# Kernel optimization log

Measured on AMD Instinct MI355X. Metric: run time of the kernel, lower is better.

The kernel has to match this reference:

```python
import jax, jax.numpy as jnp
import numpy as np

NUM_LAYER = 6
NUM_HEADS = 1
NEG_INF = -1e9


def setup_inputs() -> dict:
    key = jax.random.key(0)
    ks = jax.random.split(key, 8)
    bs, C, N = 8, 128, 2048
    H0 = (jax.random.uniform(ks[0], (bs, N, N)) < 0.2).astype(jnp.float32)
    vertex_feat = jax.random.normal(ks[1], (bs, C, N), dtype=jnp.float32)
    edge_feat = jax.random.normal(ks[2], (bs, C, N), dtype=jnp.float32)
    s = 1.0 / np.sqrt(C)  # Conv1d(k=1) default init scale
    Wq = jax.random.uniform(ks[3], (C, C), minval=-s, maxval=s, dtype=jnp.float32)
    bq = jax.random.uniform(ks[4], (C,), minval=-s, maxval=s, dtype=jnp.float32)
    Wk = jax.random.uniform(ks[5], (C, C), minval=-s, maxval=s, dtype=jnp.float32)
    bk = jax.random.uniform(ks[6], (C,), minval=-s, maxval=s, dtype=jnp.float32)
    return {"H0": H0, "vertex_feat": vertex_feat, "edge_feat": edge_feat,
            "Wq": Wq, "bq": bq, "Wk": Wk, "bk": bk, "it": 4}


def reference(H0, vertex_feat, edge_feat, Wq, bq, Wk, bk, it):
    bs, N, _ = H0.shape
    C = Wq.shape[0]
    head = NUM_HEADS
    dh = C // head
    # Conv1d kernel_size=1 == pointwise linear over channel dim
    Q = (jnp.einsum('oc,bcn->bon', Wq, vertex_feat) + bq[None, :, None]).reshape(bs, head, dh, N)
    K = (jnp.einsum('oc,bcn->bon', Wk, edge_feat) + bk[None, :, None]).reshape(bs, head, dh, N)
    att = jnp.einsum('bhco,bhci->bhoi', Q, K) / np.sqrt(dh)  # [bs,h,N,N]
    mask = jnp.where(H0 > 0, 0.0, NEG_INF)                   # masked_fill(1-H0)
    score = jax.nn.sigmoid(att + mask[:, None]).sum(axis=1) / head  # [bs,N,N]
    # mask_score, choice='topk': keep top-k scores per row
    k = round(N * 0.1 * (NUM_LAYER - 1 - it))
    topk_vals = jax.lax.top_k(score, k)[0]          # [bs,N,k]
    a_min = topk_vals[..., -1:]                     # k-th largest per row
    W = jnp.where(score >= a_min, score, 0.0)
    H = jnp.where(W > 0, H0, 0.0)
    # degree-normalization matrices (diag_embed of 1/deg, inf -> 0)
    deg_E = H.sum(axis=1)   # [bs,N] edge degrees
    deg_V = H.sum(axis=2)   # [bs,N] vertex degrees
    De_n_1 = jax.vmap(jnp.diag)(jnp.where(deg_E != 0, 1.0 / deg_E, 0.0))
    Dv_n_1 = jax.vmap(jnp.diag)(jnp.where(deg_V != 0, 1.0 / deg_V, 0.0))
    # edge weights: L2-normalized column sums of W (F.normalize, eps=1e-12)
    W_edge = W.sum(axis=1)
    nrm = jnp.maximum(jnp.linalg.norm(W_edge, axis=1, keepdims=True), 1e-12)
    W_edge = (W_edge / nrm)[:, :, None]  # [bs,N,1]
    return H, W, De_n_1, Dv_n_1, W_edge
```

## Files before the change

kernel.cpp:

```cpp
#include <hip/hip_runtime.h>
#include <math.h>

#define NUM_LAYER 6

typedef __attribute__((ext_vector_type(8))) short short8;
typedef __attribute__((ext_vector_type(4))) float f32x4;
typedef unsigned short u16;

__device__ __forceinline__ void split3(float x, u16& h, u16& m, u16& l) {
  unsigned ux = __float_as_uint(x);
  h = (u16)(ux >> 16);
  float r1 = x - __uint_as_float(ux & 0xFFFF0000u);
  unsigned u1 = __float_as_uint(r1);
  m = (u16)(u1 >> 16);
  float r2 = r1 - __uint_as_float(u1 & 0xFFFF0000u);
  l = (u16)(__float_as_uint(r2) >> 16);
}

__global__ __launch_bounds__(256) void qk_gemm_split(
    const float* __restrict__ Wq, const float* __restrict__ bq,
    const float* __restrict__ vf,
    const float* __restrict__ Wk, const float* __restrict__ bk,
    const float* __restrict__ ef,
    u16* __restrict__ Qh, u16* __restrict__ Qm, u16* __restrict__ Ql,
    u16* __restrict__ Kh, u16* __restrict__ Km, u16* __restrict__ Kl,
    int C, int N, int bs) {
  int which = (int)blockIdx.y >= bs;
  int b = (int)blockIdx.y - (which ? bs : 0);
  const float* Wm = which ? Wk : Wq;
  const float* bias = which ? bk : bq;
  const float* X = (which ? ef : vf) + (size_t)b * C * N;
  u16* Ph = which ? Kh : Qh;
  u16* Pm = which ? Km : Qm;
  u16* Pl = which ? Kl : Ql;
  int n0 = blockIdx.x * 128;
  __shared__ float As[8][128];
  __shared__ float Xs[8][128];
  int t = threadIdx.x;
  int tx = t & 15, ty = t >> 4;
  int ao = t >> 1, ac = (t & 1) * 4;
  int lk = t >> 5, lj = (t & 31) * 4;
  float acc[8][8] = {};
  for (int c0 = 0; c0 < C; c0 += 8) {
    __syncthreads();
    float4 wv = *(const float4*)&Wm[(size_t)ao * C + c0 + ac];
    As[ac + 0][ao] = wv.x; As[ac + 1][ao] = wv.y;
    As[ac + 2][ao] = wv.z; As[ac + 3][ao] = wv.w;
    *(float4*)&Xs[lk][lj] = *(const float4*)&X[(size_t)(c0 + lk) * N + n0 + lj];
    __syncthreads();
#pragma unroll
    for (int kk = 0; kk < 8; ++kk) {
      float a[8], bb[8];
      *(float4*)&a[0]  = *(const float4*)&As[kk][ty * 4];
      *(float4*)&a[4]  = *(const float4*)&As[kk][64 + ty * 4];
      *(float4*)&bb[0] = *(const float4*)&Xs[kk][tx * 4];
      *(float4*)&bb[4] = *(const float4*)&Xs[kk][64 + tx * 4];
#pragma unroll
      for (int i = 0; i < 8; ++i)
#pragma unroll
        for (int j = 0; j < 8; ++j)
          acc[i][j] = fmaf(a[i], bb[j], acc[i][j]);
    }
  }
  float bv[8];
#pragma unroll
  for (int i = 0; i < 8; ++i) bv[i] = bias[(i >> 2) * 64 + ty * 4 + (i & 3)];
#pragma unroll
  for (int j = 0; j < 8; ++j) {
    int n = n0 + tx * 4 + (j & 3) + (j >> 2) * 64;
    size_t nb = ((size_t)b * N + n) * C;
#pragma unroll
    for (int g = 0; g < 2; ++g) {
      int r0 = g * 64 + ty * 4;
      ushort4 hv, mv, lv;
      split3(acc[g * 4 + 0][j] + bv[g * 4 + 0], hv.x, mv.x, lv.x);
      split3(acc[g * 4 + 1][j] + bv[g * 4 + 1], hv.y, mv.y, lv.y);
      split3(acc[g * 4 + 2][j] + bv[g * 4 + 2], hv.z, mv.z, lv.z);
      split3(acc[g * 4 + 3][j] + bv[g * 4 + 3], hv.w, mv.w, lv.w);
      *(ushort4*)&Ph[nb + r0] = hv;
      *(ushort4*)&Pm[nb + r0] = mv;
      *(ushort4*)&Pl[nb + r0] = lv;
    }
  }
}

__global__ __launch_bounds__(256) void att_mfma(
    const u16* __restrict__ Qh, const u16* __restrict__ Qm,
    const u16* __restrict__ Ql, const u16* __restrict__ Kh,
    const u16* __restrict__ Km, const u16* __restrict__ Kl,
    const float* __restrict__ H0, float* __restrict__ score,
    int C, int N, float rsdh) {
  int b = blockIdx.z;
  int o0 = blockIdx.y * 128, i0 = blockIdx.x * 128;
  __shared__ u16 sm[6][128][40];
  __shared__ float et[4][16][68];
  int t = threadIdx.x;
  int wave = t >> 6, lane = t & 63, quad = lane >> 4, lr = lane & 15;
  int wo = wave >> 1, wi = wave & 1;
  f32x4 acc[4][4];
#pragma unroll
  for (int mi = 0; mi < 4; ++mi)
#pragma unroll
    for (int ni = 0; ni < 4; ++ni) acc[mi][ni] = (f32x4){0.f, 0.f, 0.f, 0.f};

  int ro = t >> 1, ch = (t & 1) * 16;
  size_t qbase = ((size_t)b * N + o0 + ro) * C + ch;
  size_t kbase = ((size_t)b * N + i0 + ro) * C + ch;
  const u16* gq[3] = {Qh, Qm, Ql};
  const u16* gk[3] = {Kh, Km, Kl};

  for (int c0 = 0; c0 < C; c0 += 32) {
    __syncthreads();
#pragma unroll
    for (int a = 0; a < 3; ++a) {
      const uint4* src = (const uint4*)(gq[a] + qbase + c0);
      *(uint4*)&sm[a][ro][ch] = src[0];
      *(uint4*)&sm[a][ro][ch + 8] = src[1];
      const uint4* srk = (const uint4*)(gk[a] + kbase + c0);
      *(uint4*)&sm[3 + a][ro][ch] = srk[0];
      *(uint4*)&sm[3 + a][ro][ch + 8] = srk[1];
    }
    __syncthreads();
    short8 bh[4], bm[4], bl[4];
#pragma unroll
    for (int ni = 0; ni < 4; ++ni) {
      int row = wi * 64 + ni * 16 + lr;
      bh[ni] = *(const short8*)&sm[3][row][quad * 8];
      bm[ni] = *(const short8*)&sm[4][row][quad * 8];
      bl[ni] = *(const short8*)&sm[5][row][quad * 8];
    }
#pragma unroll
    for (int mi = 0; mi < 4; ++mi) {
      int row = wo * 64 + mi * 16 + lr;
      short8 ah = *(const short8*)&sm[0][row][quad * 8];
      short8 am = *(const short8*)&sm[1][row][quad * 8];
      short8 al = *(const short8*)&sm[2][row][quad * 8];
#pragma unroll
      for (int ni = 0; ni < 4; ++ni) {
        f32x4 c = acc[mi][ni];
        c = __builtin_amdgcn_mfma_f32_16x16x32_bf16(ah, bl[ni], c, 0, 0, 0);
        c = __builtin_amdgcn_mfma_f32_16x16x32_bf16(al, bh[ni], c, 0, 0, 0);
        c = __builtin_amdgcn_mfma_f32_16x16x32_bf16(am, bm[ni], c, 0, 0, 0);
        c = __builtin_amdgcn_mfma_f32_16x16x32_bf16(ah, bm[ni], c, 0, 0, 0);
        c = __builtin_amdgcn_mfma_f32_16x16x32_bf16(am, bh[ni], c, 0, 0, 0);
        c = __builtin_amdgcn_mfma_f32_16x16x32_bf16(ah, bh[ni], c, 0, 0, 0);
        acc[mi][ni] = c;
      }
    }
  }
  const float* Hb = H0 + (size_t)b * N * N;
  float* Sb = score + (size_t)b * N * N;
  int rr = lane >> 2, seg = lane & 3;
#pragma unroll
  for (int mi = 0; mi < 4; ++mi) {
#pragma unroll
    for (int ni = 0; ni < 4; ++ni)
#pragma unroll
      for (int r = 0; r < 4; ++r)
        et[wave][quad * 4 + r][ni * 16 + lr] = acc[mi][ni][r];
    __syncthreads();
    int o = o0 + wo * 64 + mi * 16 + rr;
    const float* hr = Hb + (size_t)o * N + i0 + wi * 64;
    float* sr = Sb + (size_t)o * N + i0 + wi * 64;
#pragma unroll
    for (int j = 0; j < 4; ++j) {
      int col = j * 16 + seg * 4;
      float4 c = *(const float4*)&et[wave][rr][col];
      float4 h = *(const float4*)&hr[col];
      float4 oV;
      oV.x = (h.x > 0.f) ? 1.f / (1.f + __expf(-c.x * rsdh)) : 0.f;
      oV.y = (h.y > 0.f) ? 1.f / (1.f + __expf(-c.y * rsdh)) : 0.f;
      oV.z = (h.z > 0.f) ? 1.f / (1.f + __expf(-c.z * rsdh)) : 0.f;
      oV.w = (h.w > 0.f) ? 1.f / (1.f + __expf(-c.w * rsdh)) : 0.f;
      *(float4*)&sr[col] = oV;
    }
    __syncthreads();
  }
}

template <int V4>
__global__ __launch_bounds__(512) void topk_select(
    float* __restrict__ scoreW, float* __restrict__ Hout,
    float* __restrict__ degV, float* __restrict__ PE, float* __restrict__ PW,
    const int* __restrict__ itp, int N) {
  int b = blockIdx.y;
  int strip = blockIdx.x;
  int t = threadIdx.x;
  int wave = t >> 6, lane = t & 63;
  int row = strip * 8 + wave;
  size_t rowoff = ((size_t)b * N + row) * N;
  extern __shared__ float cols[];
  float* colE = cols;
  float* colW = cols + N;
  for (int i = t; i < 2 * N; i += 512) cols[i] = 0.f;

  float4 v4[V4];
#pragma unroll
  for (int q = 0; q < V4; ++q)
    v4[q] = *(const float4*)(scoreW + rowoff + 4 * lane + (q << 8));
  int itv = *itp;
  int k = (int)floor((double)N * 0.1 * (double)(NUM_LAYER - 1 - itv) + 0.5);
  unsigned lo = 0u, hi = 0x3F800000u;
  while (lo < hi) {
    unsigned mid = lo + ((hi - lo + 1u) >> 1);
    float thr = __uint_as_float(mid);
    int c = 0;
#pragma unroll
    for (int q = 0; q < V4; ++q) {
      c += (v4[q].x >= thr) ? 1 : 0;
      c += (v4[q].y >= thr) ? 1 : 0;
      c += (v4[q].z >= thr) ? 1 : 0;
      c += (v4[q].w >= thr) ? 1 : 0;
    }
#pragma unroll
    for (int off = 1; off < 64; off <<= 1) c += __shfl_xor(c, off);
    if (c >= k) lo = mid; else hi = mid - 1u;
  }
  float am = __uint_as_float(lo);
  __syncthreads();

  float rs = 0.f;
#pragma unroll
  for (int q = 0; q < V4; ++q) {
    int c0 = 4 * lane + (q << 8);
    float4 s = v4[q];
    float4 w, h;
    w.x = (s.x >= am) ? s.x : 0.f; h.x = (w.x > 0.f) ? 1.f : 0.f;
    w.y = (s.y >= am) ? s.y : 0.f; h.y = (w.y > 0.f) ? 1.f : 0.f;
    w.z = (s.z >= am) ? s.z : 0.f; h.z = (w.z > 0.f) ? 1.f : 0.f;
    w.w = (s.w >= am) ? s.w : 0.f; h.w = (w.w > 0.f) ? 1.f : 0.f;
    *(float4*)(scoreW + rowoff + c0) = w;
    *(float4*)(Hout + rowoff + c0) = h;
    rs += h.x + h.y + h.z + h.w;
    if (h.x != 0.f) { atomicAdd(&colE[c0 + 0], 1.f); atomicAdd(&colW[c0 + 0], w.x); }
    if (h.y != 0.f) { atomicAdd(&colE[c0 + 1], 1.f); atomicAdd(&colW[c0 + 1], w.y); }
    if (h.z != 0.f) { atomicAdd(&colE[c0 + 2], 1.f); atomicAdd(&colW[c0 + 2], w.z); }
    if (h.w != 0.f) { atomicAdd(&colE[c0 + 3], 1.f); atomicAdd(&colW[c0 + 3], w.w); }
  }
#pragma unroll
  for (int off = 32; off; off >>= 1) rs += __shfl_down(rs, off);
  if (lane == 0) degV[b * N + row] = rs;
  __syncthreads();
  int S = N >> 3;
  size_t pbase = ((size_t)b * S + strip) * N;
  for (int c = 4 * t; c < N; c += 2048) {
    *(float4*)(PE + pbase + c) = *(const float4*)&colE[c];
    *(float4*)(PW + pbase + c) = *(const float4*)&colW[c];
  }
}

__global__ __launch_bounds__(256) void col_reduce(
    const float* __restrict__ PE, const float* __restrict__ PW,
    float* __restrict__ degE, float* __restrict__ We, int N, int S) {
  int b = blockIdx.y;
  int col = blockIdx.x * 256 + threadIdx.x;
  float se0 = 0.f, se1 = 0.f, sw0 = 0.f, sw1 = 0.f;
  for (int s = 0; s < S; s += 4) {
    size_t o0 = ((size_t)b * S + s) * N + col;
    se0 += PE[o0];           sw0 += PW[o0];
    se1 += PE[o0 + N];       sw1 += PW[o0 + N];
    se0 += PE[o0 + 2 * (size_t)N]; sw0 += PW[o0 + 2 * (size_t)N];
    se1 += PE[o0 + 3 * (size_t)N]; sw1 += PW[o0 + 3 * (size_t)N];
  }
  degE[b * N + col] = se0 + se1;
  We[b * N + col] = sw0 + sw1;
}

__global__ __launch_bounds__(256) void dedv_fill(
    float* __restrict__ De, float* __restrict__ Dv,
    const float* __restrict__ degE, const float* __restrict__ degV, int N) {
  int arr = blockIdx.z;
  int b = blockIdx.y;
  int r0 = blockIdx.x * 8;
  float* out = (arr ? Dv : De) + (size_t)b * N * N;
  const float* deg = (arr ? degV : degE) + b * N;
  int t = threadIdx.x;
#pragma unroll
  for (int r = r0; r < r0 + 8; ++r) {
    float d = deg[r];
    float inv = (d != 0.f) ? 1.f / d : 0.f;
    size_t rowoff = (size_t)r * N;
    for (int c4 = t * 4; c4 < N; c4 += 1024) {
      float4 v = {0.f, 0.f, 0.f, 0.f};
      unsigned dd = (unsigned)(r - c4);
      if (dd < 4u) ((float*)&v)[dd] = inv;
      *(float4*)&out[rowoff + c4] = v;
    }
  }
}

__global__ __launch_bounds__(256) void wedge_norm(
    const float* __restrict__ We, float* __restrict__ out, int N) {
  int b = blockIdx.x;
  int t = threadIdx.x;
  const float* w = We + (size_t)b * N;
  float ss = 0.f;
  for (int i = t; i < N; i += 256) { float x = w[i]; ss += x * x; }
  for (int off = 32; off; off >>= 1) ss += __shfl_down(ss, off);
  __shared__ float p[4];
  if ((t & 63) == 0) p[t >> 6] = ss;
  __syncthreads();
  float tot = p[0] + p[1] + p[2] + p[3];
  float nrm = fmaxf(sqrtf(tot), 1e-12f);
  for (int i = t; i < N; i += 256) out[(size_t)b * N + i] = w[i] / nrm;
}

extern "C" void kernel_launch(void* const* d_in, const int* in_sizes, int n_in,
                              void* d_out, int out_size, void* d_ws, size_t ws_size,
                              hipStream_t stream) {
  const float* H0 = (const float*)d_in[0];
  const float* vf = (const float*)d_in[1];
  const float* ef = (const float*)d_in[2];
  const float* Wq = (const float*)d_in[3];
  const float* bq = (const float*)d_in[4];
  const float* Wk = (const float*)d_in[5];
  const float* bk = (const float*)d_in[6];
  const int* itp  = (const int*)d_in[7];

  int C = (int)(sqrt((double)in_sizes[3]) + 0.5);
  long long ratio = (long long)in_sizes[0] / in_sizes[1];
  int N = (int)(C * ratio);
  int bs = (int)(in_sizes[1] / ((long long)C * N));
  size_t bNN = (size_t)bs * N * N;
  size_t bNC = (size_t)bs * N * C;
  int S = N >> 3;
  size_t pElems = (size_t)bs * S * N;

  float* outH  = (float*)d_out;
  float* outW  = outH + bNN;
  float* outDe = outW + bNN;
  float* outDv = outDe + bNN;
  float* outWe = outDv + bNN;

  size_t bsN = (size_t)bs * N;
  float* degE = (float*)d_ws;
  float* degV = degE + bsN;
  float* We   = degV + bsN;
  u16* splits;
  float* PE;
  float* PW;
  size_t need = 3 * bsN * sizeof(float) + 6 * bNC * sizeof(u16) +
                2 * pElems * sizeof(float);
  if (ws_size >= need) {
    splits = (u16*)(We + bsN);
    PE = (float*)(splits + 6 * bNC);
    PW = PE + pElems;
  } else {
    splits = (u16*)outDe;
    PE = outDv;
    PW = PE + pElems;
  }
  u16* Qh = splits;
  u16* Qm = Qh + bNC;
  u16* Ql = Qm + bNC;
  u16* Kh = Ql + bNC;
  u16* Km = Kh + bNC;
  u16* Kl = Km + bNC;

  float rsdh = (float)(1.0 / sqrt((double)C));
  size_t colsBytes = 2 * (size_t)N * sizeof(float);

  qk_gemm_split<<<dim3(N / 128, 2 * bs), 256, 0, stream>>>(
      Wq, bq, vf, Wk, bk, ef, Qh, Qm, Ql, Kh, Km, Kl, C, N, bs);
  att_mfma<<<dim3(N / 128, N / 128, bs), 256, 0, stream>>>(
      Qh, Qm, Ql, Kh, Km, Kl, H0, outW, C, N, rsdh);
  if (N == 2048)
    topk_select<8><<<dim3(S, bs), 512, colsBytes, stream>>>(
        outW, outH, degV, PE, PW, itp, N);
  else if (N == 1024)
    topk_select<4><<<dim3(S, bs), 512, colsBytes, stream>>>(
        outW, outH, degV, PE, PW, itp, N);
  else
    topk_select<16><<<dim3(S, bs), 512, colsBytes, stream>>>(
        outW, outH, degV, PE, PW, itp, N);
  col_reduce<<<dim3(N / 256, bs), 256, 0, stream>>>(PE, PW, degE, We, N, S);
  dedv_fill<<<dim3(N / 8, bs, 2), 256, 0, stream>>>(outDe, outDv, degE,
                                                    degV, N);
  wedge_norm<<<dim3(bs), 256, 0, stream>>>(We, outWe, N);
}
```

Before: 870.1 us.

## Use ternary threshold search, fuse Dv fill into topk, widen col_reduce

The top-k threshold search now tests two split points per pass, packing both counts into one int, which cuts the number of reduction rounds by about log2(3). When the workspace is large enough, topk_select writes the diagonal Dv rows directly, so dedv_fill only produces De. col_reduce now splits the strip sum across four waves with a shared-memory combine to raise parallelism. The risks are extra compare work per pass, Dv stores competing with the topk bandwidth, and the packed counts overflowing if a row ever holds more than 65535 elements.

```diff
diff --git a/kernel.cpp b/kernel.cpp
--- a/kernel.cpp
+++ b/kernel.cpp
@@ -181,7 +181,8 @@
 template <int V4>
 __global__ __launch_bounds__(512) void topk_select(
     float* __restrict__ scoreW, float* __restrict__ Hout,
-    float* __restrict__ degV, float* __restrict__ PE, float* __restrict__ PW,
+    float* __restrict__ degV, float* __restrict__ Dv, int dodv,
+    float* __restrict__ PE, float* __restrict__ PW,
     const int* __restrict__ itp, int N) {
   int b = blockIdx.y;
   int strip = blockIdx.x;
@@ -202,19 +203,24 @@
   int k = (int)floor((double)N * 0.1 * (double)(NUM_LAYER - 1 - itv) + 0.5);
   unsigned lo = 0u, hi = 0x3F800000u;
   while (lo < hi) {
-    unsigned mid = lo + ((hi - lo + 1u) >> 1);
-    float thr = __uint_as_float(mid);
+    unsigned r = hi - lo;
+    unsigned p1 = lo + (r + 2u) / 3u;
+    unsigned p2 = lo + (2u * r + 2u) / 3u;
+    float t1 = __uint_as_float(p1), t2 = __uint_as_float(p2);
     int c = 0;
 #pragma unroll
     for (int q = 0; q < V4; ++q) {
-      c += (v4[q].x >= thr) ? 1 : 0;
-      c += (v4[q].y >= thr) ? 1 : 0;
-      c += (v4[q].z >= thr) ? 1 : 0;
-      c += (v4[q].w >= thr) ? 1 : 0;
+      c += (v4[q].x >= t1) ? 1 : 0; c += (v4[q].x >= t2) ? 0x10000 : 0;
+      c += (v4[q].y >= t1) ? 1 : 0; c += (v4[q].y >= t2) ? 0x10000 : 0;
+      c += (v4[q].z >= t1) ? 1 : 0; c += (v4[q].z >= t2) ? 0x10000 : 0;
+      c += (v4[q].w >= t1) ? 1 : 0; c += (v4[q].w >= t2) ? 0x10000 : 0;
     }
 #pragma unroll
     for (int off = 1; off < 64; off <<= 1) c += __shfl_xor(c, off);
-    if (c >= k) lo = mid; else hi = mid - 1u;
+    int c2 = c >> 16, c1 = c & 0xFFFF;
+    if (c2 >= k) lo = p2;
+    else if (c1 >= k) { lo = p1; hi = p2 - 1u; }
+    else hi = p1 - 1u;
   }
   float am = __uint_as_float(lo);
   __syncthreads();
@@ -239,7 +245,18 @@
   }
 #pragma unroll
   for (int off = 32; off; off >>= 1) rs += __shfl_down(rs, off);
-  if (lane == 0) degV[b * N + row] = rs;
+  float rsb = __shfl(rs, 0);
+  if (lane == 0) degV[b * N + row] = rsb;
+  if (dodv) {
+    float inv = (rsb != 0.f) ? 1.f / rsb : 0.f;
+    float* dvr = Dv + ((size_t)b * N + row) * N;
+    for (int c4 = lane * 4; c4 < N; c4 += 256) {
+      float4 z = {0.f, 0.f, 0.f, 0.f};
+      unsigned dd = (unsigned)(row - c4);
+      if (dd < 4u) ((float*)&z)[dd] = inv;
+      *(float4*)&dvr[c4] = z;
+    }
+  }
   __syncthreads();
   int S = N >> 3;
   size_t pbase = ((size_t)b * S + strip) * N;
@@ -253,17 +270,27 @@
     const float* __restrict__ PE, const float* __restrict__ PW,
     float* __restrict__ degE, float* __restrict__ We, int N, int S) {
   int b = blockIdx.y;
-  int col = blockIdx.x * 256 + threadIdx.x;
-  float se0 = 0.f, se1 = 0.f, sw0 = 0.f, sw1 = 0.f;
-  for (int s = 0; s < S; s += 4) {
-    size_t o0 = ((size_t)b * S + s) * N + col;
-    se0 += PE[o0];           sw0 += PW[o0];
-    se1 += PE[o0 + N];       sw1 += PW[o0 + N];
-    se0 += PE[o0 + 2 * (size_t)N]; sw0 += PW[o0 + 2 * (size_t)N];
-    se1 += PE[o0 + 3 * (size_t)N]; sw1 += PW[o0 + 3 * (size_t)N];
-  }
-  degE[b * N + col] = se0 + se1;
-  We[b * N + col] = sw0 + sw1;
+  int l = threadIdx.x & 63;
+  int sg = threadIdx.x >> 6;
+  int col = blockIdx.x * 64 + l;
+  int cnt = S >> 2;
+  int s0 = sg * cnt;
+  float se = 0.f, sw = 0.f;
+  for (int i = 0; i < cnt; ++i) {
+    size_t o = ((size_t)b * S + s0 + i) * N + col;
+    se += PE[o];
+    sw += PW[o];
+  }
+  __shared__ float rE[4][64], rW[4][64];
+  rE[sg][l] = se;
+  rW[sg][l] = sw;
+  __syncthreads();
+  if (sg == 0) {
+    float te = rE[0][l] + rE[1][l] + rE[2][l] + rE[3][l];
+    float tw = rW[0][l] + rW[1][l] + rW[2][l] + rW[3][l];
+    degE[b * N + col] = te;
+    We[b * N + col] = tw;
+  }
 }
 
 __global__ __launch_bounds__(256) void dedv_fill(
@@ -339,16 +366,19 @@
   u16* splits;
   float* PE;
   float* PW;
+  int dodv;
   size_t need = 3 * bsN * sizeof(float) + 6 * bNC * sizeof(u16) +
                 2 * pElems * sizeof(float);
   if (ws_size >= need) {
     splits = (u16*)(We + bsN);
     PE = (float*)(splits + 6 * bNC);
     PW = PE + pElems;
+    dodv = 1;
   } else {
     splits = (u16*)outDe;
     PE = outDv;
     PW = PE + pElems;
+    dodv = 0;
   }
   u16* Qh = splits;
   u16* Qm = Qh + bNC;
@@ -366,15 +396,15 @@
       Qh, Qm, Ql, Kh, Km, Kl, H0, outW, C, N, rsdh);
   if (N == 2048)
     topk_select<8><<<dim3(S, bs), 512, colsBytes, stream>>>(
-        outW, outH, degV, PE, PW, itp, N);
+        outW, outH, degV, outDv, dodv, PE, PW, itp, N);
   else if (N == 1024)
     topk_select<4><<<dim3(S, bs), 512, colsBytes, stream>>>(
-        outW, outH, degV, PE, PW, itp, N);
+        outW, outH, degV, outDv, dodv, PE, PW, itp, N);
   else
     topk_select<16><<<dim3(S, bs), 512, colsBytes, stream>>>(
-        outW, outH, degV, PE, PW, itp, N);
-  col_reduce<<<dim3(N / 256, bs), 256, 0, stream>>>(PE, PW, degE, We, N, S);
-  dedv_fill<<<dim3(N / 8, bs, 2), 256, 0, stream>>>(outDe, outDv, degE,
-                                                    degV, N);
+        outW, outH, degV, outDv, dodv, PE, PW, itp, N);
+  col_reduce<<<dim3(N / 64, bs), 256, 0, stream>>>(PE, PW, degE, We, N, S);
+  dedv_fill<<<dim3(N / 8, bs, dodv ? 1 : 2), 256, 0, stream>>>(
+      outDe, outDv, degE, degV, N);
   wedge_norm<<<dim3(bs), 256, 0, stream>>>(We, outWe, N);
 }
```

Result: no change. 861.7 us (-1.0%).
